# Kernel tuning notes

Measured on AMD Instinct MI355X. Metric: run time of the kernel, lower is better.

Reference implementation:

```python
import jax, jax.numpy as jnp
import numpy as np

B, N, I, O, R = 8, 1024, 256, 256, 8


def setup_inputs() -> dict:
    key = jax.random.key(0)
    k1, k2, k3 = jax.random.split(key, 3)
    x = jax.random.normal(k1, (B, N, I), dtype=jnp.float32)
    adj = jax.random.uniform(k2, (B, N, N, R), dtype=jnp.float32)  # soft adjacency [b, src, dst, r]
    weight = jax.random.normal(k3, (R, I, O), dtype=jnp.float32)   # per-relation transform
    return {"x": x, "adj": adj, "weight": weight}


def reference(x, adj, weight):
    # per-relation transformed features: [b, src, r, o]
    f = jnp.einsum('bni,rio->bnro', x, weight)
    # contraction over source nodes and relations, weighted by soft adjacency:
    # out[b, dst, o] = sum_{src, r} adj[b, src, dst, r] * f[b, src, r, o]
    out = jnp.einsum('bnro,bnmr->bmo', f, adj)
    # normalization: total incoming soft-edge weight per destination node
    denom = jnp.clip(adj.sum(axis=(1, 3)), 1e-16, None)  # [b, dst]
    return out / denom[..., None]
```

## Files before the change

### kernel.cpp

```cpp
#include <hip/hip_runtime.h>
#include <stdint.h>


typedef float          floatx4  __attribute__((ext_vector_type(4)));
typedef short          shortx8  __attribute__((ext_vector_type(8)));
typedef unsigned short ushortx4 __attribute__((ext_vector_type(4)));
typedef unsigned short ushortx8 __attribute__((ext_vector_type(8)));

__device__ __forceinline__ unsigned short f2bf(float f) {
  union { float f; unsigned int u; } v; v.f = f;
  unsigned int u = v.u + 0x7FFFu + ((v.u >> 16) & 1u);
  return (unsigned short)(u >> 16);
}

__device__ __forceinline__ void gload16(const void* g, void* l) {
  __builtin_amdgcn_global_load_lds((__attribute__((address_space(1))) void*)g,
                                   (__attribute__((address_space(3))) void*)l,
                                   16, 0, 0);
}

__global__ __launch_bounds__(256) void prep_xw(const float* __restrict__ x,
                                               const float* __restrict__ w,
                                               unsigned short* __restrict__ xbf,
                                               unsigned short* __restrict__ wt) {
  int bid = blockIdx.x;
  if (bid < 1024) {
    int t = bid * 256 + threadIdx.x;
    const float4* p = (const float4*)x + (size_t)t * 2;
    float4 a = p[0], b4 = p[1];
    ushortx8 o;
    o[0] = f2bf(a.x);  o[1] = f2bf(a.y);  o[2] = f2bf(a.z);  o[3] = f2bf(a.w);
    o[4] = f2bf(b4.x); o[5] = f2bf(b4.y); o[6] = f2bf(b4.z); o[7] = f2bf(b4.w);
    *(ushortx8*)(xbf + (size_t)t * 8) = o;
  } else {
    int id = (bid - 1024) * 256 + threadIdx.x;
    int r = id >> 16, i = (id >> 8) & 255, o = id & 255;
    float v = w[((size_t)(r * 256 + i) << 8) + o];
    wt[((size_t)(o * 8 + r) << 8) + i] = f2bf(v);
  }
}

__global__ __launch_bounds__(256) void k1_gemm(const unsigned short* __restrict__ xbf,
                                               const unsigned short* __restrict__ wt,
                                               unsigned short* __restrict__ ft) {
  int bid = blockIdx.x;
  int p0 = (bid & 15) * 128, q0 = (bid >> 4) * 128;
  int l = threadIdx.x & 63, w = threadIdx.x >> 6;
  int lr = l & 15, lg = l >> 4;
  int pw = p0 + (w >> 1) * 64, qw = q0 + (w & 1) * 64;

  floatx4 acc[4][4] = {};
#pragma unroll
  for (int ks = 0; ks < 8; ++ks) {
    shortx8 a[4], b[4];
#pragma unroll
    for (int pi = 0; pi < 4; ++pi)
      a[pi] = *(const shortx8*)(wt + (size_t)(pw + pi * 16 + lr) * 256 + ks * 32 + lg * 8);
#pragma unroll
    for (int qi = 0; qi < 4; ++qi)
      b[qi] = *(const shortx8*)(xbf + (size_t)(qw + qi * 16 + lr) * 256 + ks * 32 + lg * 8);
#pragma unroll
    for (int pi = 0; pi < 4; ++pi)
#pragma unroll
      for (int qi = 0; qi < 4; ++qi)
        acc[pi][qi] = __builtin_amdgcn_mfma_f32_16x16x32_bf16(a[pi], b[qi], acc[pi][qi], 0, 0, 0);
  }
#pragma unroll
  for (int pi = 0; pi < 4; ++pi) {
    int nbase = pw + pi * 16 + lg * 4;
    int o = nbase >> 3, rb = nbase & 7;
#pragma unroll
    for (int qi = 0; qi < 4; ++qi) {
      int m = qw + qi * 16 + lr;
      int b8 = m >> 10, src = m & 1023;
      ushortx4 h;
      h[0] = f2bf(acc[pi][qi][0]); h[1] = f2bf(acc[pi][qi][1]);
      h[2] = f2bf(acc[pi][qi][2]); h[3] = f2bf(acc[pi][qi][3]);
      *(ushortx4*)(ft + ((size_t)(b8 * 256 + o) << 13) + src * 8 + rb) = h;
    }
  }
}

#define BSZ (64 * 64)
#define ASZ (32 * 64)
#define NKT 128
__global__ __launch_bounds__(256, 4) void k2_gemm(const float* __restrict__ adj,
                                                  const unsigned short* __restrict__ ft,
                                                  float* __restrict__ outp) {
  __shared__ __align__(16) unsigned short Blds[2 * BSZ];
  __shared__ __align__(16) unsigned short Alds[2 * ASZ];

  int bid = blockIdx.x;
  int b = bid & 7;
  int o0 = ((bid >> 3) & 3) * 64;
  int dst0 = (bid >> 5) * 32;

  int t = threadIdx.x, l = t & 63, w = t >> 6;
  int lr = l & 15, lg = l >> 4;

  int dst_l = l >> 1;
  int rh = (l & 1) * 4;
  int csw = (l & 7) ^ (l >> 3);

  const size_t adj_b = (size_t)b << 23;
  const unsigned short* ftb = ft + ((size_t)b << 21);

  float dsum = 0.f;
  floatx4 acc[2] = {};
  float4 av[2];

  auto A_load = [&](int kt, float4* v) {
#pragma unroll
    for (int j = 0; j < 2; ++j) {
      int src = kt * 8 + w + j * 4;
      v[j] = *(const float4*)(adj + adj_b + ((size_t)src << 13)
                              + ((size_t)(dst0 + dst_l) << 3) + rh);
    }
  };
  auto A_store = [&](int buf, const float4* v) {
#pragma unroll
    for (int j = 0; j < 2; ++j) {
      int src_l = w + j * 4;
      float4 q = v[j];
      dsum += q.x + q.y + q.z + q.w;
      ushortx4 h;
      h[0] = f2bf(q.x); h[1] = f2bf(q.y); h[2] = f2bf(q.z); h[3] = f2bf(q.w);
      int slot = src_l ^ (dst_l & 7);
      *(ushortx4*)&Alds[buf * ASZ + dst_l * 64 + slot * 8 + rh] = h;
    }
  };
  auto B_stage = [&](int kt, int buf) {
    int kbase = kt * 64;
#pragma unroll
    for (int i = 0; i < 2; ++i) {
      int orow = w * 16 + i * 8 + (l >> 3);
      const unsigned short* g = ftb + ((size_t)(o0 + orow) << 13) + kbase + (csw << 3);
      gload16(g, &Blds[buf * BSZ + (w * 16 + i * 8) * 64]);
    }
  };
  auto compute = [&](int buf) {
#pragma unroll
    for (int s = 0; s < 2; ++s) {
      int slotbase = s * 4 + lg;
      shortx8 af[2];
#pragma unroll
      for (int mi = 0; mi < 2; ++mi) {
        int arow = mi * 16 + lr;
        af[mi] = *(const shortx8*)&Alds[buf * ASZ + arow * 64 + ((slotbase ^ (arow & 7)) << 3)];
      }
      int brow = w * 16 + lr;
      shortx8 bfr = *(const shortx8*)&Blds[buf * BSZ + brow * 64 + ((slotbase ^ (lr & 7)) << 3)];
#pragma unroll
      for (int mi = 0; mi < 2; ++mi)
        acc[mi] = __builtin_amdgcn_mfma_f32_16x16x32_bf16(af[mi], bfr, acc[mi], 0, 0, 0);
    }
  };

  A_load(0, av);
  B_stage(0, 0);
  A_store(0, av);
  __syncthreads();

  for (int kt = 0; kt < NKT; ++kt) {
    int cur = kt & 1, nxt = cur ^ 1;
    bool has = (kt + 1) < NKT;
    if (has) { A_load(kt + 1, av); B_stage(kt + 1, nxt); }
    compute(cur);
    if (has) A_store(nxt, av);
    __syncthreads();
  }

  float* dsf = (float*)Alds;
  dsf[t] = dsum;
  __syncthreads();
  if (t < 32) {
    float s = 0.f;
#pragma unroll
    for (int sl = 0; sl < 4; ++sl) {
      s += dsf[sl * 64 + t * 2];
      s += dsf[sl * 64 + t * 2 + 1];
    }
    dsf[256 + t] = s;
  }
  __syncthreads();

#pragma unroll
  for (int mi = 0; mi < 2; ++mi) {
#pragma unroll
    for (int reg = 0; reg < 4; ++reg) {
      int rowl = mi * 16 + lg * 4 + reg;
      float dinv = 1.f / fmaxf(dsf[256 + rowl], 1e-16f);
      int row = dst0 + rowl;
      int col = o0 + w * 16 + lr;
      outp[(((size_t)b << 10) + row) * 256 + col] = acc[mi][reg] * dinv;
    }
  }
}

extern "C" void kernel_launch(void* const* d_in, const int* in_sizes, int n_in,
                              void* d_out, int out_size, void* d_ws, size_t ws_size,
                              hipStream_t stream) {
  const float* x   = (const float*)d_in[0];
  const float* adj = (const float*)d_in[1];
  const float* w   = (const float*)d_in[2];
  float* out = (float*)d_out;

  char* ws = (char*)d_ws;
  unsigned short* ft  = (unsigned short*)(ws);
  unsigned short* xbf = (unsigned short*)(ws + 33554432);
  unsigned short* wt  = (unsigned short*)(ws + 37748736);

  prep_xw<<<3072, 256, 0, stream>>>(x, w, xbf, wt);
  k1_gemm<<<1024, 256, 0, stream>>>(xbf, wt, ft);
  k2_gemm<<<1024, 256, 0, stream>>>(adj, ft, out);
}
```

Before: 166.9 us.

## Triple-buffer k2 LDS tiles with two-stage-ahead prefetch and partial vmcnt waits

Moves the adjacency/feature GEMM kernel from double buffering to a three-slot LDS ring. Global loads for tile kt+2 are issued while tile kt is computed, and the converted A tile for kt+1 is stored to LDS in the same step. The full __syncthreads is replaced by an s_waitcnt that keeps four vector loads outstanding, followed by a raw barrier, so the next tile's loads need not drain at every step. This raises LDS use per block, which may limit occupancy, and relies on the hand-counted vmcnt matching the number of loads in flight.

```diff
diff --git a/kernel.cpp b/kernel.cpp
--- a/kernel.cpp
+++ b/kernel.cpp
@@ -18,6 +18,10 @@
                                    (__attribute__((address_space(3))) void*)l,
                                    16, 0, 0);
 }
+
+#define FENCE_KEEP4 asm volatile("s_waitcnt vmcnt(4) lgkmcnt(0)" ::: "memory")
+#define FENCE_ALL   asm volatile("s_waitcnt vmcnt(0) lgkmcnt(0)" ::: "memory")
+#define MEMFENCE    asm volatile("" ::: "memory")
 
 __global__ __launch_bounds__(256) void prep_xw(const float* __restrict__ x,
                                                const float* __restrict__ w,
@@ -87,8 +91,8 @@
 __global__ __launch_bounds__(256, 4) void k2_gemm(const float* __restrict__ adj,
                                                   const unsigned short* __restrict__ ft,
                                                   float* __restrict__ outp) {
-  __shared__ __align__(16) unsigned short Blds[2 * BSZ];
-  __shared__ __align__(16) unsigned short Alds[2 * ASZ];
+  __shared__ __align__(16) unsigned short Blds[3 * BSZ];
+  __shared__ __align__(16) unsigned short Alds[3 * ASZ];
 
   int bid = blockIdx.x;
   int b = bid & 7;
@@ -107,7 +111,7 @@
 
   float dsum = 0.f;
   floatx4 acc[2] = {};
-  float4 av[2];
+  float4 avA[2], avB[2];
 
   auto A_load = [&](int kt, float4* v) {
 #pragma unroll
@@ -156,19 +160,32 @@
     }
   };
 
-  A_load(0, av);
   B_stage(0, 0);
-  A_store(0, av);
+  A_load(0, avA);
+  A_load(1, avB);
+  B_stage(1, 1);
+  A_store(0, avA);
+  avA[0] = avB[0]; avA[1] = avB[1];
+  FENCE_KEEP4;
+  __builtin_amdgcn_s_barrier();
+  MEMFENCE;
+
+  int c0 = 0, c1 = 1, c2 = 2;
+  for (int kt = 0; kt < NKT; ++kt) {
+    bool iss = (kt + 2) < NKT;
+    bool st  = (kt + 1) < NKT;
+    if (iss) { A_load(kt + 2, avB); B_stage(kt + 2, c2); }
+    if (st)  A_store(c1, avA);
+    compute(c0);
+    if (st) {
+      if (iss) { FENCE_KEEP4; } else { FENCE_ALL; }
+      __builtin_amdgcn_s_barrier();
+      MEMFENCE;
+    }
+    avA[0] = avB[0]; avA[1] = avB[1];
+    int tmp = c0; c0 = c1; c1 = c2; c2 = tmp;
+  }
   __syncthreads();
-
-  for (int kt = 0; kt < NKT; ++kt) {
-    int cur = kt & 1, nxt = cur ^ 1;
-    bool has = (kt + 1) < NKT;
-    if (has) { A_load(kt + 1, av); B_stage(kt + 1, nxt); }
-    compute(cur);
-    if (has) A_store(nxt, av);
-    __syncthreads();
-  }
 
   float* dsf = (float*)Alds;
   dsf[t] = dsum;
```

New measurement: 161.9 us. -3.0%, faster.
